# Performance work log

Measured on AMD Instinct MI355X. Metric: run time of the kernel, lower is better.

Reference implementation:

```python
import jax, jax.numpy as jnp
import numpy as np
from jax import lax

B, N, C = 4, 4096, 512
NUM_HEADS = 8
HD = C // NUM_HEADS  # 64, equals L
L = 64               # H = W = L, N = L*L


def setup_inputs() -> dict:
    key = jax.random.key(0)
    ks = jax.random.split(key, 8)
    d = HD
    return {
        "x": jax.random.normal(ks[0], (B, N, C), jnp.float32),
        "log_peak_width": jnp.log(jnp.float32(3.0)),
        "log_valley_width": jnp.log(jnp.float32(3.0)),
        "w_qkv": jax.random.normal(ks[1], (3 * C, C), jnp.float32) * 0.02,
        "b_qkv": jnp.zeros((3 * C,), jnp.float32),
        "w_proj": jax.random.normal(ks[2], (C, C), jnp.float32) * 0.02,
        "b_proj": jnp.zeros((C,), jnp.float32),
        "omega": jnp.linspace(0.1, 10.0, d // 2).astype(jnp.float32),
        "w_pp1": jax.random.normal(ks[3], (2 * d, 1, 3), jnp.float32) * 0.3,   # grouped conv, groups=d
        "b_pp1": jnp.zeros((2 * d,), jnp.float32),
        "w_pp2": jax.random.normal(ks[4], (d, 2 * d, 1), jnp.float32) * 0.1,
        "b_pp2": jnp.zeros((d,), jnp.float32),
        "w_gate": jax.random.normal(ks[5], (d, d, 1), jnp.float32) * 0.1,
        "b_gate": jnp.zeros((d,), jnp.float32),
    }


def _spectral_gate(x_spec, log_pw, log_vw):
    # x_spec: [B, C, N]. torch nonzero flattens (b,c,i) -> use per-position counts
    # (exactly equivalent to summing one gaussian per nonzero occurrence).
    n = x_spec.shape[-1]
    sc = jnp.sign(jnp.diff(jnp.diff(x_spec, axis=-1), axis=-1))       # [B,C,N-2]
    peak_cnt = jnp.sum(sc < 0, axis=(0, 1)).astype(x_spec.dtype)      # [N-2]
    valley_cnt = jnp.sum(sc > 0, axis=(0, 1)).astype(x_spec.dtype)    # [N-2]
    pos = jnp.arange(n, dtype=x_spec.dtype)
    centers = jnp.arange(1, n - 1, dtype=x_spec.dtype)                # index i+1

    def gsum(cnt, logw):
        dist = (pos[None, :] - centers[:, None]) * jnp.exp(-logw)     # [N-2, N]
        return cnt @ jnp.exp(-dist * dist)                            # [N]

    attn = gsum(peak_cnt, log_pw) + gsum(valley_cnt, log_vw)
    return (attn - attn.min()) / (attn.max() - attn.min() + 1e-6)     # [N], uniform over (B,C)


def _spectral_pe(omega, w1, b1, w2, b2, wg, bg, l, d):
    grid = jnp.arange(l, dtype=jnp.float32)
    rel = grid[:, None] - grid[None, :]                               # [l,l]
    freqs = rel[..., None] * omega                                    # [l,l,d/2]
    pe = jnp.concatenate([jnp.sin(freqs), jnp.cos(freqs)], axis=-1)   # [l,l,d]
    pe = pe.reshape(l * l, d).T[None]                                 # [1,d,l*l]
    dn = ('NCH', 'OIH', 'NCH')
    h = lax.conv_general_dilated(pe, w1, (1,), [(1, 1)], dimension_numbers=dn,
                                 feature_group_count=d) + b1[None, :, None]
    h = jax.nn.gelu(h, approximate=False)
    pe2 = (lax.conv_general_dilated(h, w2, (1,), [(0, 0)],
                                    dimension_numbers=dn) + b2[None, :, None])[0]  # [d, l*l]
    gate = jax.nn.sigmoid(wg[:, :, 0] @ pe2.mean(-1, keepdims=True) + bg[:, None])  # [d,1]
    pe3 = pe2.T.reshape(l, l, d)
    # torch rearrange '(l1 l2) d -> l1 l2 d' on [d,1] gate: reshape to [l, d//l, 1] and broadcast
    return pe3 * gate.reshape(l, d // l, 1)


def _rope(t, pe, d):
    b, h, n, _ = t.shape
    l = pe.shape[0]
    tr = t.reshape(b, h, l, l, d)
    tr = tr + tr * pe * (d ** -0.25)
    return tr.reshape(b, h, n, d)


def reference(x, log_peak_width, log_valley_width, w_qkv, b_qkv, w_proj, b_proj,
              omega, w_pp1, b_pp1, w_pp2, b_pp2, w_gate, b_gate):
    b, n, c = x.shape
    h, d = NUM_HEADS, HD
    gate = _spectral_gate(x.transpose(0, 2, 1), log_peak_width, log_valley_width)  # [n]
    xg = x * gate[None, :, None]
    qkv = xg @ w_qkv.T + b_qkv                                        # [b,n,3c]
    q, k, v = jnp.split(qkv, 3, axis=-1)
    tohead = lambda t: t.reshape(b, n, h, d).transpose(0, 2, 1, 3)    # [b,h,n,d]
    q, k, v = tohead(q), tohead(k), tohead(v)
    q = jax.nn.elu(q) + 1.0
    k = jax.nn.elu(k) + 1.0
    pe = _spectral_pe(omega, w_pp1, b_pp1, w_pp2, b_pp2, w_gate, b_gate, L, d)
    q = _rope(q, pe, d)
    k = _rope(k, pe, d)
    scale = (d * n) ** -0.5
    ctx = jnp.einsum('bhnd,bhne->bhde', q, k) * scale                 # [b,h,d,d]
    out = jnp.einsum('bhnd,bhde->bhne', v, ctx) * scale               # [b,h,n,d]
    out = out.transpose(0, 2, 1, 3).reshape(b, n, c)
    return out @ w_proj.T + b_proj
```

## Files before the change

### kernel.cpp

```cpp
#include <hip/hip_runtime.h>
#include <hip/hip_bf16.h>
#include <math.h>

constexpr int BB = 4;
constexpr int NN = 4096;
constexpr int CC = 512;
constexpr int HH = 8;
constexpr int DD = 64;
constexpr int NCNT = NN - 2;

typedef __bf16 bf16x8 __attribute__((ext_vector_type(8)));
typedef float f32x4 __attribute__((ext_vector_type(4)));

__device__ __forceinline__ float b2f(ushort u) {
  unsigned v = ((unsigned)u) << 16;
  return __builtin_bit_cast(float, v);
}
__device__ __forceinline__ ushort f2b(float f) {
  __hip_bfloat16 h = __float2bfloat16(f);
  return __builtin_bit_cast(ushort, h);
}
__device__ __forceinline__ void gload16(const ushort* g, ushort* l) {
  __builtin_amdgcn_global_load_lds(
      (const __attribute__((address_space(1))) unsigned int*)g,
      (__attribute__((address_space(3))) unsigned int*)l, 16, 0, 0);
}

__global__ __launch_bounds__(512) void k_counts_prep(
    const float* __restrict__ x, int* __restrict__ pcntP,
    int* __restrict__ pcntV, ushort* __restrict__ Xh) {
  int b = blockIdx.x >> 8;
  int tile = blockIdx.x & 255;
  int c = threadIdx.x;
  int lane = threadIdx.x & 63;
  int i0 = tile * 16;
  const float* xb = x + (size_t)b * NN * CC + c;

  float v[18];
  #pragma unroll
  for (int r = 0; r < 18; ++r) {
    int i = i0 + r;
    v[r] = xb[(size_t)(i < NN ? i : NN - 1) * CC];
  }

  #pragma unroll
  for (int r = 0; r < 16; ++r)
    Xh[((size_t)b * NN + i0 + r) * CC + c] = f2b(v[r]);

  __shared__ int redP[16], redV[16];
  if (threadIdx.x < 16) { redP[threadIdx.x] = 0; redV[threadIdx.x] = 0; }
  __syncthreads();

  #pragma unroll
  for (int r = 0; r < 16; ++r) {
    int i = i0 + r;
    if (i < NCNT) {
      float d2 = (v[r + 2] - v[r + 1]) - (v[r + 1] - v[r]);
      unsigned long long mneg = __ballot(d2 < 0.0f);
      unsigned long long mpos = __ballot(d2 > 0.0f);
      if (lane == 0) {
        atomicAdd(&redP[r], __popcll(mneg));
        atomicAdd(&redV[r], __popcll(mpos));
      }
    }
  }
  __syncthreads();
  if (threadIdx.x < 16) {
    int i = i0 + threadIdx.x;
    pcntP[b * NN + i] = (i < NCNT) ? redP[threadIdx.x] : 0;
    pcntV[b * NN + i] = (i < NCNT) ? redV[threadIdx.x] : 0;
  }
}

__global__ void k_etab2(const float* __restrict__ lpw, const float* __restrict__ lvw,
                        const int* __restrict__ pcntP, const int* __restrict__ pcntV,
                        float* __restrict__ etabP, float* __restrict__ etabV,
                        float* __restrict__ fcntP, float* __restrict__ fcntV) {
  int i = blockIdx.x * 256 + threadIdx.x;
  float ipw = expf(-lpw[0]);
  float ivw = expf(-lvw[0]);
  float t1 = (float)i * ipw;
  float t2 = (float)i * ivw;
  etabP[i] = expf(-t1 * t1);
  etabV[i] = expf(-t2 * t2);
  fcntP[i] = (float)(pcntP[i] + pcntP[NN + i] + pcntP[2 * NN + i] + pcntP[3 * NN + i]);
  fcntV[i] = (float)(pcntV[i] + pcntV[NN + i] + pcntV[2 * NN + i] + pcntV[3 * NN + i]);
}

__global__ void k_gsum(const float* __restrict__ fcntP, const float* __restrict__ fcntV,
                       const float* __restrict__ etabP, const float* __restrict__ etabV,
                       float* __restrict__ attn) {
  int p = blockIdx.x;
  int tid = threadIdx.x;
  float acc = 0.f;
  for (int i = tid; i < NCNT; i += 256) {
    int a = p - 1 - i;
    a = a < 0 ? -a : a;
    acc += fcntP[i] * etabP[a] + fcntV[i] * etabV[a];
  }
  __shared__ float red[256];
  red[tid] = acc;
  __syncthreads();
  for (int s = 128; s > 0; s >>= 1) {
    if (tid < s) red[tid] += red[tid + s];
    __syncthreads();
  }
  if (tid == 0) attn[p] = red[0];
}

__global__ void k_norm(const float* __restrict__ attn, float* __restrict__ gate) {
  int tid = threadIdx.x;
  float v0 = attn[tid], v1 = attn[tid + 1024], v2 = attn[tid + 2048], v3 = attn[tid + 3072];
  float mn = fminf(fminf(v0, v1), fminf(v2, v3));
  float mx = fmaxf(fmaxf(v0, v1), fmaxf(v2, v3));
  __shared__ float rmn[1024], rmx[1024];
  rmn[tid] = mn; rmx[tid] = mx;
  __syncthreads();
  for (int s = 512; s > 0; s >>= 1) {
    if (tid < s) {
      rmn[tid] = fminf(rmn[tid], rmn[tid + s]);
      rmx[tid] = fmaxf(rmx[tid], rmx[tid + s]);
    }
    __syncthreads();
  }
  float lo = rmn[0];
  float denom = rmx[0] - rmn[0] + 1e-6f;
  gate[tid]        = (v0 - lo) / denom;
  gate[tid + 1024] = (v1 - lo) / denom;
  gate[tid + 2048] = (v2 - lo) / denom;
  gate[tid + 3072] = (v3 - lo) / denom;
}

__global__ __launch_bounds__(256) void k_pe(
    const float* __restrict__ omega,
    const float* __restrict__ w1, const float* __restrict__ b1,
    const float* __restrict__ w2, const float* __restrict__ b2,
    float* __restrict__ pe2) {
  int g = threadIdx.x >> 6;
  int j = threadIdx.x & 63;
  int n = blockIdx.x * 4 + g;
  __shared__ float pec[4][3][64];
  __shared__ float hs[4][128];
  for (int t = 0; t < 3; ++t) {
    int m = n + t - 1;
    float v = 0.f;
    if (m >= 0 && m < NN) {
      int l1 = m >> 6, l2 = m & 63;
      float rel = (float)(l1 - l2);
      v = (j < 32) ? sinf(rel * omega[j]) : cosf(rel * omega[j - 32]);
    }
    pec[g][t][j] = v;
  }
  __syncthreads();
  for (int o = j; o < 128; o += 64) {
    int ci = o >> 1;
    float hv = b1[o];
    #pragma unroll
    for (int t = 0; t < 3; ++t) hv += pec[g][t][ci] * w1[o * 3 + t];
    hv = 0.5f * hv * (1.f + erff(hv * 0.70710678118654752f));
    hs[g][o] = hv;
  }
  __syncthreads();
  float acc = b2[j];
  for (int o = 0; o < 128; ++o) acc += hs[g][o] * w2[j * 128 + o];
  pe2[(size_t)j * NN + n] = acc;
}

__global__ void k_gatepe(const float* __restrict__ pe2,
                         const float* __restrict__ wg, const float* __restrict__ bg,
                         float* __restrict__ gpe) {
  int tid = threadIdx.x;
  int j = tid & 63, part = tid >> 6;
  float s = 0.f;
  const float* row = pe2 + (size_t)j * NN + part * 1024;
  for (int t = 0; t < 1024; ++t) s += row[t];
  __shared__ float ps[4][64];
  __shared__ float mean[64];
  ps[part][j] = s;
  __syncthreads();
  if (tid < 64) mean[j] = (ps[0][j] + ps[1][j] + ps[2][j] + ps[3][j]) * (1.f / 4096.f);
  __syncthreads();
  if (tid < 64) {
    float g = bg[j];
    for (int k2 = 0; k2 < 64; ++k2) g += wg[j * 64 + k2] * mean[k2];
    gpe[j] = 1.f / (1.f + expf(-g));
  }
}

__global__ void k_ropemul(const float* __restrict__ pe2, const float* __restrict__ gpe,
                          float* __restrict__ ropem) {
  int idx = blockIdx.x * 256 + threadIdx.x;
  int n = idx >> 6, dd = idx & 63;
  ropem[idx] = 1.f + pe2[(size_t)dd * NN + n] * gpe[n >> 6] * 0.35355339059327373f;
}

__global__ void k_prep_h(const float* __restrict__ src,
                         ushort* __restrict__ Sh, int nelem) {
  int idx4 = (blockIdx.x * 256 + threadIdx.x) * 4;
  if (idx4 >= nelem) return;
  float4 v = *(const float4*)&src[idx4];
  ushort4 h;
  ((ushort*)&h)[0] = f2b(v.x);
  ((ushort*)&h)[1] = f2b(v.y);
  ((ushort*)&h)[2] = f2b(v.z);
  ((ushort*)&h)[3] = f2b(v.w);
  *(ushort4*)&Sh[idx4] = h;
}

__global__ __launch_bounds__(256) void k_prep_wvt(const float* __restrict__ wqkv,
                                                  ushort* __restrict__ Wvth,
                                                  ushort* __restrict__ Wvtl) {
  int bx = blockIdx.x & 7;
  int by = blockIdx.x >> 3;
  __shared__ float t[64][65];
  int tid = threadIdx.x;
  #pragma unroll
  for (int it = 0; it < 4; ++it) {
    int idx = tid + it * 256;
    int r = idx >> 4;
    int c4 = (idx & 15) * 4;
    float4 v = *(const float4*)&wqkv[(size_t)(1024 + by * 64 + r) * 512 + bx * 64 + c4];
    t[r][c4] = v.x; t[r][c4 + 1] = v.y; t[r][c4 + 2] = v.z; t[r][c4 + 3] = v.w;
  }
  __syncthreads();
  #pragma unroll
  for (int it = 0; it < 4; ++it) {
    int idx = tid + it * 256;
    int r = idx >> 4;
    int c4 = (idx & 15) * 4;
    ushort4 h4, l4;
    #pragma unroll
    for (int q = 0; q < 4; ++q) {
      float v = t[c4 + q][r];
      ushort hi = f2b(v);
      ((ushort*)&h4)[q] = hi;
      ((ushort*)&l4)[q] = f2b(v - b2f(hi));
    }
    size_t o = (size_t)(bx * 64 + r) * 512 + by * 64 + c4;
    *(ushort4*)&Wvth[o] = h4;
    *(ushort4*)&Wvtl[o] = l4;
  }
}

template <int BTERMS, int EPI>
__global__ __launch_bounds__(256) void k_gemm_t(
    const ushort* __restrict__ Ag, const ushort* __restrict__ Bgh,
    const ushort* __restrict__ Bgl,
    const float* __restrict__ bias, const float* __restrict__ gate,
    const float* __restrict__ ropem,
    float* __restrict__ outF, ushort* __restrict__ qT, ushort* __restrict__ kT,
    int ntn, int ncols) {
  const int nwg = gridDim.x;
  const int hw = blockIdx.x;
  const int logical = (hw & 7) * (nwg >> 3) + (hw >> 3);
  const int m0 = (logical / ntn) * 128, n0 = (logical % ntn) * 128;

  const int tid = threadIdx.x, wave = tid >> 6, lane = tid & 63;
  const int wm = wave >> 1, wn = wave & 1;
  __shared__ ushort sA[2][4096];
  __shared__ ushort sB[2][BTERMS * 4096];
  f32x4 acc[4][4] = {};

  const int lr = lane >> 2;
  const int ci = lane & 3;
  const int scol = (ci ^ ((lr >> 1) & 3)) * 8;
  const int rA = lane & 15;
  const int cswz = ((lane >> 4) ^ ((rA >> 1) & 3)) * 8;

  const int chunk0 = wave * 2, chunk1 = wave * 2 + 1;
  const int row0 = chunk0 * 16 + lr, row1 = chunk1 * 16 + lr;

  const ushort* Bh_ = Bgh + (EPI == 2 ? (size_t)(m0 >> 12) * 262144 : 0);
  const ushort* Bl_ = (BTERMS == 2)
      ? (Bgl + (EPI == 2 ? (size_t)(m0 >> 12) * 262144 : 0)) : nullptr;

#define STAGE(T, S)                                                        \
  {                                                                        \
    const int k0s = (T) * 32;                                              \
    size_t ga0 = (size_t)(m0 + row0) * CC + k0s + scol;                    \
    size_t ga1 = (size_t)(m0 + row1) * CC + k0s + scol;                    \
    size_t gb0 = (size_t)(n0 + row0) * CC + k0s + scol;                    \
    size_t gb1 = (size_t)(n0 + row1) * CC + k0s + scol;                    \
    gload16(Ag + ga0, &sA[S][chunk0 * 512]);                               \
    gload16(Ag + ga1, &sA[S][chunk1 * 512]);                               \
    gload16(Bh_ + gb0, &sB[S][chunk0 * 512]);                              \
    gload16(Bh_ + gb1, &sB[S][chunk1 * 512]);                              \
    if (BTERMS == 2) {                                                     \
      gload16(Bl_ + gb0, &sB[S][4096 + chunk0 * 512]);                     \
      gload16(Bl_ + gb1, &sB[S][4096 + chunk1 * 512]);                     \
    }                                                                      \
  }

  STAGE(0, 0);
  __syncthreads();

  for (int t = 0; t < 16; ++t) {
    if (t < 15) STAGE(t + 1, (t + 1) & 1);
    const int cur = t & 1;
    bf16x8 af[4], bh[4], bl[4];
    #pragma unroll
    for (int m = 0; m < 4; ++m)
      af[m] = *(const bf16x8*)(&sA[cur][(wm * 64 + m * 16 + rA) * 32 + cswz]);
    #pragma unroll
    for (int n = 0; n < 4; ++n) {
      int off = (wn * 64 + n * 16 + rA) * 32 + cswz;
      bh[n] = *(const bf16x8*)(&sB[cur][off]);
      if (BTERMS == 2) bl[n] = *(const bf16x8*)(&sB[cur][4096 + off]);
    }
    #pragma unroll
    for (int m = 0; m < 4; ++m)
      #pragma unroll
      for (int n = 0; n < 4; ++n) {
        acc[m][n] = __builtin_amdgcn_mfma_f32_16x16x32_bf16(af[m], bh[n], acc[m][n], 0, 0, 0);
        if (BTERMS == 2)
          acc[m][n] = __builtin_amdgcn_mfma_f32_16x16x32_bf16(af[m], bl[n], acc[m][n], 0, 0, 0);
      }
    __syncthreads();
  }
#undef STAGE

  const int kj = lane >> 4, l15 = lane & 15;
  #pragma unroll
  for (int m = 0; m < 4; ++m) {
    #pragma unroll
    for (int n = 0; n < 4; ++n) {
      if (EPI == 2) {
        #pragma unroll
        for (int r = 0; r < 4; ++r) {
          int row = m0 + wm * 64 + m * 16 + kj * 4 + r;
          int col = n0 + wn * 64 + n * 16 + l15;
          int nseq = row & (NN - 1), b = row >> 12;
          float val = acc[m][n][r] * gate[nseq] + bias[b * 512 + col];
          outF[(size_t)row * ncols + col] = val;
        }
      } else if (EPI == 3) {
        #pragma unroll
        for (int r = 0; r < 4; ++r) {
          int row = m0 + wm * 64 + m * 16 + kj * 4 + r;
          int col = n0 + wn * 64 + n * 16 + l15;
          qT[(size_t)row * ncols + col] = f2b(acc[m][n][r]);
        }
      } else {
        int rowb = m0 + wm * 64 + m * 16 + kj * 4;
        int col = n0 + wn * 64 + n * 16 + l15;
        int nseqb = rowb & (NN - 1), b = rowb >> 12;
        int part = col >> 9, h = (col >> 6) & 7, dd = col & 63;
        ushort4 pk;
        #pragma unroll
        for (int r = 0; r < 4; ++r) {
          int nseq = nseqb + r;
          float val = acc[m][n][r] * gate[nseq] + bias[col];
          float e = val > 0.f ? val + 1.f : expf(val);
          ((ushort*)&pk)[r] = f2b(e * ropem[nseq * 64 + dd]);
        }
        ushort* dst = (part == 0 ? qT : kT) +
                      ((size_t)(b * HH + h) * DD + dd) * NN + nseqb;
        *(ushort4*)dst = pk;
      }
    }
  }
}

__global__ __launch_bounds__(256) void k_ctx_mfma(
    const ushort* __restrict__ qT, const ushort* __restrict__ kT,
    float* __restrict__ ctxp) {
  int blk = blockIdx.x;
  int bh = blk >> 4, chunk = blk & 15;
  int wave = threadIdx.x >> 6, lane = threadIdx.x & 63;
  int l15 = lane & 15, kj = lane >> 4;
  const size_t base = (size_t)bh * DD * NN;
  const int n0 = chunk * 256 + wave * 64;
  f32x4 acc[4][4] = {};
  #pragma unroll
  for (int ks = 0; ks < 2; ++ks) {
    const int nb = n0 + ks * 32 + kj * 8;
    bf16x8 qa[4], ka[4];
    #pragma unroll
    for (int m = 0; m < 4; ++m)
      qa[m] = *(const bf16x8*)(qT + base + (size_t)(m * 16 + l15) * NN + nb);
    #pragma unroll
    for (int n = 0; n < 4; ++n)
      ka[n] = *(const bf16x8*)(kT + base + (size_t)(n * 16 + l15) * NN + nb);
    #pragma unroll
    for (int m = 0; m < 4; ++m)
      #pragma unroll
      for (int n = 0; n < 4; ++n)
        acc[m][n] = __builtin_amdgcn_mfma_f32_16x16x32_bf16(qa[m], ka[n], acc[m][n], 0, 0, 0);
  }
  __shared__ float red[4][4096];
  #pragma unroll
  for (int m = 0; m < 4; ++m)
    #pragma unroll
    for (int n = 0; n < 4; ++n)
      #pragma unroll
      for (int r = 0; r < 4; ++r)
        red[wave][(m * 16 + kj * 4 + r) * 64 + n * 16 + l15] = acc[m][n][r];
  __syncthreads();
  const float scale = 1.f / 512.f;
  float* dst = ctxp + (size_t)(bh * 16 + chunk) * 4096;
  #pragma unroll
  for (int e = 0; e < 16; ++e) {
    int idx = threadIdx.x + e * 256;
    float s = red[0][idx] + red[1][idx] + red[2][idx] + red[3][idx];
    dst[idx] = s * scale;
  }
}

__global__ void k_ctx_red(const float* __restrict__ ctxp, float* __restrict__ ctx) {
  int idx = blockIdx.x * 256 + threadIdx.x;
  int bh = idx >> 12, off = idx & 4095;
  float s = 0.f;
  #pragma unroll
  for (int c2 = 0; c2 < 16; ++c2)
    s += ctxp[((size_t)bh * 16 + c2) * 4096 + off];
  ctx[idx] = s;
}

__global__ __launch_bounds__(256) void k_mproj(
    const float* __restrict__ ctx, const float* __restrict__ wp,
    ushort* __restrict__ Mfh, ushort* __restrict__ Mfl) {
  int blk = blockIdx.x;
  int b = blk >> 6, h = (blk >> 3) & 7, oq = blk & 7;
  int tid = threadIdx.x;
  int o = oq * 64 + (tid & 63);
  int d0 = (tid >> 6) * 16;
  __shared__ float cs[64][64];
  #pragma unroll
  for (int it = 0; it < 4; ++it) {
    int idx = (tid + 256 * it) * 4;
    *(float4*)&cs[idx >> 6][idx & 63] =
        *(const float4*)&ctx[(size_t)(b * 8 + h) * 4096 + idx];
  }
  __syncthreads();
  float wv[64];
  #pragma unroll
  for (int e = 0; e < 64; ++e) wv[e] = wp[(size_t)o * 512 + h * 64 + e];
  for (int d = d0; d < d0 + 16; ++d) {
    float s = 0.f;
    #pragma unroll
    for (int e = 0; e < 64; ++e) s += cs[d][e] * wv[e];
    s *= (1.f / 512.f);
    ushort hi = f2b(s);
    size_t idx = ((size_t)b * 512 + o) * 512 + h * 64 + d;
    Mfh[idx] = hi;
    Mfl[idx] = f2b(s - b2f(hi));
  }
}

__global__ void k_beff(const ushort* __restrict__ Mfh, const ushort* __restrict__ Mfl,
                       const float* __restrict__ bqkv,
                       const float* __restrict__ bproj, float* __restrict__ beff) {
  int w = threadIdx.x >> 6, lane = threadIdx.x & 63;
  int t = blockIdx.x * 4 + w;
  int b = t >> 9, o = t & 511;
  size_t base = ((size_t)b * 512 + o) * 512;
  float s = 0.f;
  #pragma unroll
  for (int c = 0; c < 512; c += 64) {
    float m = b2f(Mfh[base + c + lane]) + b2f(Mfl[base + c + lane]);
    s += bqkv[1024 + c + lane] * m;
  }
  #pragma unroll
  for (int off = 32; off > 0; off >>= 1) s += __shfl_down(s, off);
  if (lane == 0) beff[t] = s + bproj[o];
}

extern "C" void kernel_launch(void* const* d_in, const int* in_sizes, int n_in,
                              void* d_out, int out_size, void* d_ws, size_t ws_size,
                              hipStream_t stream) {
  const float* x    = (const float*)d_in[0];
  const float* lpw  = (const float*)d_in[1];
  const float* lvw  = (const float*)d_in[2];
  const float* wqkv = (const float*)d_in[3];
  const float* bqkv = (const float*)d_in[4];
  const float* wproj= (const float*)d_in[5];
  const float* bproj= (const float*)d_in[6];
  const float* omega= (const float*)d_in[7];
  const float* w1   = (const float*)d_in[8];
  const float* b1   = (const float*)d_in[9];
  const float* w2   = (const float*)d_in[10];
  const float* b2   = (const float*)d_in[11];
  const float* wg   = (const float*)d_in[12];
  const float* bg   = (const float*)d_in[13];
  float* out = (float*)d_out;

  constexpr size_t MB = 1024 * 1024;
  char* w = (char*)d_ws;
  int*   pcntP  = (int*)(w);
  int*   pcntV  = (int*)(w + 64 * 1024);
  float* attn   = (float*)(w + 128 * 1024);
  float* gate   = (float*)(w + 144 * 1024);
  float* etabP  = (float*)(w + 160 * 1024);
  float* etabV  = (float*)(w + 176 * 1024);
  float* fcntP  = (float*)(w + 192 * 1024);
  float* fcntV  = (float*)(w + 208 * 1024);
  float* pe2    = (float*)(w + 256 * 1024);
  float* gpe    = (float*)(w + 1280 * 1024);
  float* ropem  = (float*)(w + 1344 * 1024);
  ushort* Xh    = (ushort*)(w + 4 * MB);
  ushort* qT    = (ushort*)(w + 20 * MB);
  ushort* kT    = (ushort*)(w + 36 * MB);
  ushort* Whqk  = (ushort*)(w + 52 * MB);
  ushort* Wvth  = (ushort*)(w + 53 * MB);
  ushort* Wvtl  = (ushort*)(w + 53 * MB + 512 * 1024);
  ushort* Mfh   = (ushort*)(w + 54 * MB);
  ushort* Mfl   = (ushort*)(w + 56 * MB);
  ushort* G2h   = (ushort*)(w + 58 * MB);
  float* beff   = (float*)(w + 60 * MB);
  float* ctxp   = (float*)(w + 61 * MB);
  float* ctx    = (float*)(w + 69 * MB);

  k_counts_prep<<<BB * 256, 512, 0, stream>>>(x, pcntP, pcntV, Xh);
  k_etab2<<<16, 256, 0, stream>>>(lpw, lvw, pcntP, pcntV, etabP, etabV, fcntP, fcntV);
  k_gsum<<<NN, 256, 0, stream>>>(fcntP, fcntV, etabP, etabV, attn);
  k_norm<<<1, 1024, 0, stream>>>(attn, gate);
  k_pe<<<1024, 256, 0, stream>>>(omega, w1, b1, w2, b2, pe2);
  k_gatepe<<<1, 256, 0, stream>>>(pe2, wg, bg, gpe);
  k_ropemul<<<1024, 256, 0, stream>>>(pe2, gpe, ropem);
  k_prep_h<<<512, 256, 0, stream>>>(wqkv, Whqk, 1024 * CC);
  k_prep_wvt<<<64, 256, 0, stream>>>(wqkv, Wvth, Wvtl);

  k_gemm_t<1, 1><<<1024, 256, 0, stream>>>(Xh, Whqk, nullptr, bqkv, gate, ropem,
                                           nullptr, qT, kT, 8, 0);
  k_ctx_mfma<<<512, 256, 0, stream>>>(qT, kT, ctxp);
  k_ctx_red<<<512, 256, 0, stream>>>(ctxp, ctx);
  k_mproj<<<256, 256, 0, stream>>>(ctx, wproj, Mfh, Mfl);
  k_gemm_t<2, 3><<<64, 256, 0, stream>>>(Mfh, Wvth, Wvtl, nullptr, nullptr,
                                         nullptr, nullptr, G2h, nullptr, 4, 512);
  k_beff<<<512, 256, 0, stream>>>(Mfh, Mfl, bqkv, bproj, beff);

  k_gemm_t<1, 2><<<512, 256, 0, stream>>>(Xh, G2h, nullptr, beff, gate, nullptr,
                                          out, nullptr, nullptr, 4, CC);
}
```

Baseline: 190.5 us.

## Use 256-row, 8-wave GEMM tiles for QK and output projections

```diff
diff --git a/kernel.cpp b/kernel.cpp
--- a/kernel.cpp
+++ b/kernel.cpp
@@ -242,24 +242,25 @@
   }
 }
 
-template <int BTERMS, int EPI>
-__global__ __launch_bounds__(256) void k_gemm_t(
+template <int BN, int EPI>
+__global__ __launch_bounds__(512) void k_gemm8(
     const ushort* __restrict__ Ag, const ushort* __restrict__ Bgh,
-    const ushort* __restrict__ Bgl,
     const float* __restrict__ bias, const float* __restrict__ gate,
     const float* __restrict__ ropem,
     float* __restrict__ outF, ushort* __restrict__ qT, ushort* __restrict__ kT,
     int ntn, int ncols) {
+  constexpr int NF = BN / 32;
+  constexpr int BCH = BN / 16;
   const int nwg = gridDim.x;
   const int hw = blockIdx.x;
   const int logical = (hw & 7) * (nwg >> 3) + (hw >> 3);
-  const int m0 = (logical / ntn) * 128, n0 = (logical % ntn) * 128;
+  const int m0 = (logical / ntn) * 256, n0 = (logical % ntn) * BN;
 
   const int tid = threadIdx.x, wave = tid >> 6, lane = tid & 63;
   const int wm = wave >> 1, wn = wave & 1;
-  __shared__ ushort sA[2][4096];
-  __shared__ ushort sB[2][BTERMS * 4096];
-  f32x4 acc[4][4] = {};
+  __shared__ ushort sA[2][8192];
+  __shared__ ushort sB[2][BN * 32];
+  f32x4 acc[4][NF] = {};
 
   const int lr = lane >> 2;
   const int ci = lane & 3;
@@ -267,54 +268,41 @@
   const int rA = lane & 15;
   const int cswz = ((lane >> 4) ^ ((rA >> 1) & 3)) * 8;
 
-  const int chunk0 = wave * 2, chunk1 = wave * 2 + 1;
-  const int row0 = chunk0 * 16 + lr, row1 = chunk1 * 16 + lr;
-
+  const ushort* pA0 = Ag + (size_t)(m0 + (2 * wave) * 16 + lr) * CC + scol;
+  const ushort* pA1 = Ag + (size_t)(m0 + (2 * wave + 1) * 16 + lr) * CC + scol;
   const ushort* Bh_ = Bgh + (EPI == 2 ? (size_t)(m0 >> 12) * 262144 : 0);
-  const ushort* Bl_ = (BTERMS == 2)
-      ? (Bgl + (EPI == 2 ? (size_t)(m0 >> 12) * 262144 : 0)) : nullptr;
+  const ushort* pB0 = Bh_ + (size_t)(n0 + wave * 16 + lr) * CC + scol;
 
 #define STAGE(T, S)                                                        \
   {                                                                        \
-    const int k0s = (T) * 32;                                              \
-    size_t ga0 = (size_t)(m0 + row0) * CC + k0s + scol;                    \
-    size_t ga1 = (size_t)(m0 + row1) * CC + k0s + scol;                    \
-    size_t gb0 = (size_t)(n0 + row0) * CC + k0s + scol;                    \
-    size_t gb1 = (size_t)(n0 + row1) * CC + k0s + scol;                    \
-    gload16(Ag + ga0, &sA[S][chunk0 * 512]);                               \
-    gload16(Ag + ga1, &sA[S][chunk1 * 512]);                               \
-    gload16(Bh_ + gb0, &sB[S][chunk0 * 512]);                              \
-    gload16(Bh_ + gb1, &sB[S][chunk1 * 512]);                              \
-    if (BTERMS == 2) {                                                     \
-      gload16(Bl_ + gb0, &sB[S][4096 + chunk0 * 512]);                     \
-      gload16(Bl_ + gb1, &sB[S][4096 + chunk1 * 512]);                     \
+    gload16(pA0 + (T) * 32, &sA[S][(2 * wave) * 512]);                     \
+    gload16(pA1 + (T) * 32, &sA[S][(2 * wave + 1) * 512]);                 \
+    if (BCH == 8) {                                                        \
+      gload16(pB0 + (T) * 32, &sB[S][wave * 512]);                         \
+    } else {                                                               \
+      if (wave < BCH) gload16(pB0 + (T) * 32, &sB[S][wave * 512]);         \
     }                                                                      \
   }
 
   STAGE(0, 0);
   __syncthreads();
 
+  #pragma unroll
   for (int t = 0; t < 16; ++t) {
     if (t < 15) STAGE(t + 1, (t + 1) & 1);
     const int cur = t & 1;
-    bf16x8 af[4], bh[4], bl[4];
+    bf16x8 af[4], bhf[NF];
     #pragma unroll
     for (int m = 0; m < 4; ++m)
       af[m] = *(const bf16x8*)(&sA[cur][(wm * 64 + m * 16 + rA) * 32 + cswz]);
     #pragma unroll
-    for (int n = 0; n < 4; ++n) {
-      int off = (wn * 64 + n * 16 + rA) * 32 + cswz;
-      bh[n] = *(const bf16x8*)(&sB[cur][off]);
-      if (BTERMS == 2) bl[n] = *(const bf16x8*)(&sB[cur][4096 + off]);
-    }
+    for (int n = 0; n < NF; ++n)
+      bhf[n] = *(const bf16x8*)(&sB[cur][(wn * (BN / 2) + n * 16 + rA) * 32 + cswz]);
     #pragma unroll
     for (int m = 0; m < 4; ++m)
       #pragma unroll
-      for (int n = 0; n < 4; ++n) {
-        acc[m][n] = __builtin_amdgcn_mfma_f32_16x16x32_bf16(af[m], bh[n], acc[m][n], 0, 0, 0);
-        if (BTERMS == 2)
-          acc[m][n] = __builtin_amdgcn_mfma_f32_16x16x32_bf16(af[m], bl[n], acc[m][n], 0, 0, 0);
-      }
+      for (int n = 0; n < NF; ++n)
+        acc[m][n] = __builtin_amdgcn_mfma_f32_16x16x32_bf16(af[m], bhf[n], acc[m][n], 0, 0, 0);
     __syncthreads();
   }
 #undef STAGE
@@ -323,26 +311,19 @@
   #pragma unroll
   for (int m = 0; m < 4; ++m) {
     #pragma unroll
-    for (int n = 0; n < 4; ++n) {
+    for (int n = 0; n < NF; ++n) {
       if (EPI == 2) {
         #pragma unroll
         for (int r = 0; r < 4; ++r) {
           int row = m0 + wm * 64 + m * 16 + kj * 4 + r;
-          int col = n0 + wn * 64 + n * 16 + l15;
+          int col = n0 + wn * (BN / 2) + n * 16 + l15;
           int nseq = row & (NN - 1), b = row >> 12;
           float val = acc[m][n][r] * gate[nseq] + bias[b * 512 + col];
           outF[(size_t)row * ncols + col] = val;
         }
-      } else if (EPI == 3) {
-        #pragma unroll
-        for (int r = 0; r < 4; ++r) {
-          int row = m0 + wm * 64 + m * 16 + kj * 4 + r;
-          int col = n0 + wn * 64 + n * 16 + l15;
-          qT[(size_t)row * ncols + col] = f2b(acc[m][n][r]);
-        }
       } else {
         int rowb = m0 + wm * 64 + m * 16 + kj * 4;
-        int col = n0 + wn * 64 + n * 16 + l15;
+        int col = n0 + wn * (BN / 2) + n * 16 + l15;
         int nseqb = rowb & (NN - 1), b = rowb >> 12;
         int part = col >> 9, h = (col >> 6) & 7, dd = col & 63;
         ushort4 pk;
@@ -359,6 +340,85 @@
       }
     }
   }
+}
+
+__global__ __launch_bounds__(256) void k_gemm_g2(
+    const ushort* __restrict__ Ag, const ushort* __restrict__ Bgh,
+    const ushort* __restrict__ Bgl, ushort* __restrict__ outB, int ntn) {
+  const int nwg = gridDim.x;
+  const int hw = blockIdx.x;
+  const int logical = (hw & 7) * (nwg >> 3) + (hw >> 3);
+  const int m0 = (logical / ntn) * 128, n0 = (logical % ntn) * 128;
+
+  const int tid = threadIdx.x, wave = tid >> 6, lane = tid & 63;
+  const int wm = wave >> 1, wn = wave & 1;
+  __shared__ ushort sA[2][4096];
+  __shared__ ushort sB[2][8192];
+  f32x4 acc[4][4] = {};
+
+  const int lr = lane >> 2;
+  const int ci = lane & 3;
+  const int scol = (ci ^ ((lr >> 1) & 3)) * 8;
+  const int rA = lane & 15;
+  const int cswz = ((lane >> 4) ^ ((rA >> 1) & 3)) * 8;
+
+  const int chunk0 = wave * 2, chunk1 = wave * 2 + 1;
+  const ushort* pA0 = Ag + (size_t)(m0 + chunk0 * 16 + lr) * CC + scol;
+  const ushort* pA1 = Ag + (size_t)(m0 + chunk1 * 16 + lr) * CC + scol;
+  const ushort* pB0 = Bgh + (size_t)(n0 + chunk0 * 16 + lr) * CC + scol;
+  const ushort* pB1 = Bgh + (size_t)(n0 + chunk1 * 16 + lr) * CC + scol;
+  const ushort* pB0l = Bgl + (size_t)(n0 + chunk0 * 16 + lr) * CC + scol;
+  const ushort* pB1l = Bgl + (size_t)(n0 + chunk1 * 16 + lr) * CC + scol;
+
+#define STAGE(T, S)                                                        \
+  {                                                                        \
+    gload16(pA0 + (T) * 32, &sA[S][chunk0 * 512]);                         \
+    gload16(pA1 + (T) * 32, &sA[S][chunk1 * 512]);                         \
+    gload16(pB0 + (T) * 32, &sB[S][chunk0 * 512]);                         \
+    gload16(pB1 + (T) * 32, &sB[S][chunk1 * 512]);                         \
+    gload16(pB0l + (T) * 32, &sB[S][4096 + chunk0 * 512]);                 \
+    gload16(pB1l + (T) * 32, &sB[S][4096 + chunk1 * 512]);                 \
+  }
+
+  STAGE(0, 0);
+  __syncthreads();
+
+  #pragma unroll
+  for (int t = 0; t < 16; ++t) {
+    if (t < 15) STAGE(t + 1, (t + 1) & 1);
+    const int cur = t & 1;
+    bf16x8 af[4], bh[4], bl[4];
+    #pragma unroll
+    for (int m = 0; m < 4; ++m)
+      af[m] = *(const bf16x8*)(&sA[cur][(wm * 64 + m * 16 + rA) * 32 + cswz]);
+    #pragma unroll
+    for (int n = 0; n < 4; ++n) {
+      int off = (wn * 64 + n * 16 + rA) * 32 + cswz;
+      bh[n] = *(const bf16x8*)(&sB[cur][off]);
+      bl[n] = *(const bf16x8*)(&sB[cur][4096 + off]);
+    }
+    #pragma unroll
+    for (int m = 0; m < 4; ++m)
+      #pragma unroll
+      for (int n = 0; n < 4; ++n) {
+        acc[m][n] = __builtin_amdgcn_mfma_f32_16x16x32_bf16(af[m], bh[n], acc[m][n], 0, 0, 0);
+        acc[m][n] = __builtin_amdgcn_mfma_f32_16x16x32_bf16(af[m], bl[n], acc[m][n], 0, 0, 0);
+      }
+    __syncthreads();
+  }
+#undef STAGE
+
+  const int kj = lane >> 4, l15 = lane & 15;
+  #pragma unroll
+  for (int m = 0; m < 4; ++m)
+    #pragma unroll
+    for (int n = 0; n < 4; ++n)
+      #pragma unroll
+      for (int r = 0; r < 4; ++r) {
+        int row = m0 + wm * 64 + m * 16 + kj * 4 + r;
+        int col = n0 + wn * 64 + n * 16 + l15;
+        outB[(size_t)row * 512 + col] = f2b(acc[m][n][r]);
+      }
 }
 
 __global__ __launch_bounds__(256) void k_ctx_mfma(
@@ -520,15 +580,14 @@
   k_prep_h<<<512, 256, 0, stream>>>(wqkv, Whqk, 1024 * CC);
   k_prep_wvt<<<64, 256, 0, stream>>>(wqkv, Wvth, Wvtl);
 
-  k_gemm_t<1, 1><<<1024, 256, 0, stream>>>(Xh, Whqk, nullptr, bqkv, gate, ropem,
+  k_gemm8<128, 1><<<512, 512, 0, stream>>>(Xh, Whqk, bqkv, gate, ropem,
                                            nullptr, qT, kT, 8, 0);
   k_ctx_mfma<<<512, 256, 0, stream>>>(qT, kT, ctxp);
   k_ctx_red<<<512, 256, 0, stream>>>(ctxp, ctx);
   k_mproj<<<256, 256, 0, stream>>>(ctx, wproj, Mfh, Mfl);
-  k_gemm_t<2, 3><<<64, 256, 0, stream>>>(Mfh, Wvth, Wvtl, nullptr, nullptr,
-                                         nullptr, nullptr, G2h, nullptr, 4, 512);
+  k_gemm_g2<<<64, 256, 0, stream>>>(Mfh, Wvth, Wvtl, G2h, 4);
   k_beff<<<512, 256, 0, stream>>>(Mfh, Mfl, bqkv, bproj, beff);
 
-  k_gemm_t<1, 2><<<512, 256, 0, stream>>>(Xh, G2h, nullptr, beff, gate, nullptr,
-                                          out, nullptr, nullptr, 4, CC);
-}
+  k_gemm8<64, 2><<<512, 512, 0, stream>>>(Xh, G2h, beff, gate, nullptr,
+                                          out, nullptr, nullptr, 8, 512);
+}
```

After: 178.7 us. 1.07x faster.
